# Kernel tuning notes

Measured on AMD Instinct MI355X. Metric: run time of the kernel, lower is better.

## Reference

```python
import jax, jax.numpy as jnp
import numpy as np

WS = (5, 5, 5, 5)  # 4D window

def _rel_index(ws):
    # faithful port of WindowAttention.relative_bias_4d
    coords = np.stack(np.meshgrid(*[np.arange(w) for w in ws], indexing='ij'))  # (4, H,W,Hs,Ws)
    flat = coords.reshape(len(ws), -1)                       # (4, N)
    rel = (flat[:, :, None] - flat[:, None, :]).transpose(1, 2, 0).astype(np.int64)  # (N, N, 4)
    rel = rel + np.array([ws[0] - 1, ws[1] - 1, ws[2] - 1, ws[3] - 1])
    rel[..., 0] *= (2 * ws[0] - 1) ** 3
    rel[..., 1] *= (2 * ws[1] - 1) ** 2
    rel[..., 2] *= (2 * ws[2] - 1)
    return rel.sum(-1)  # (N, N), values in [0, (2w-1)^4)


def setup_inputs() -> dict:
    key = jax.random.key(0)
    ks = jax.random.split(key, 7)
    dim, heads = 128, 4
    B_, nW = 64, 32
    N = 5 ** 4  # 625
    tbl = (2 * 5 - 1) ** 4  # 6561
    inp = {
        'x': jax.random.normal(ks[0], (B_, N, dim), jnp.float32),
        'mask': jax.random.normal(ks[1], (nW, N, N), jnp.float32),
        'qkv_w': jax.random.normal(ks[2], (3 * dim, dim), jnp.float32) * 0.02,
        'qkv_b': jax.random.normal(ks[3], (3 * dim,), jnp.float32) * 0.02,
        'proj_w': jax.random.normal(ks[4], (dim, dim), jnp.float32) * 0.02,
        'proj_b': jax.random.normal(ks[5], (dim,), jnp.float32) * 0.02,
        'bias_table': jax.random.normal(ks[6], (tbl, heads), jnp.float32) * 0.02,
        'rel_index': jnp.asarray(_rel_index(WS), jnp.int32),
    }
    return inp


def reference(x, mask, qkv_w, qkv_b, proj_w, proj_b, bias_table, rel_index):
    B_, N, C = x.shape
    H = bias_table.shape[-1]
    D = C // H
    scale = D ** -0.5
    # qkv projection -> (3, B_, H, N, D)
    qkv = (x @ qkv_w.T + qkv_b).reshape(B_, N, 3, H, D).transpose(2, 0, 3, 1, 4)
    q, k, v = qkv[0], qkv[1], qkv[2]
    attn = jnp.einsum('bhnd,bhmd->bhnm', q * scale, k)       # (B_, H, N, N)
    bias = bias_table[rel_index].transpose(2, 0, 1)          # (H, N, N)
    attn = attn + bias[None]
    nW = mask.shape[0]
    attn = attn.reshape(B_ // nW, nW, H, N, N) + mask[None, :, None]
    attn = jax.nn.softmax(attn.reshape(B_, H, N, N), axis=-1)
    out = jnp.einsum('bhnm,bhmd->bhnd', attn, v)             # (B_, H, N, D)
    out = out.transpose(0, 2, 1, 3).reshape(B_, N, C)
    return out @ proj_w.T + proj_b
```

## Files before the change

kernel.cpp:

```cpp
#include <hip/hip_runtime.h>
#include <stdint.h>

typedef __attribute__((ext_vector_type(8))) __bf16 bf16x8;
typedef __attribute__((ext_vector_type(4))) __bf16 bf16x4;
typedef __attribute__((ext_vector_type(4))) float f32x4;

#define DEV __device__ __forceinline__
#define LOG2E 1.4426950408889634f
#define SCALE 0.17677669529663687f

static constexpr size_t OFF_Q     = 0;
static constexpr size_t OFF_K     = 10485760;
static constexpr size_t OFF_VT    = 20971520;
static constexpr size_t OFF_O     = 31457280;
static constexpr size_t OFF_BIASP = 41697280;
static constexpr size_t OFF_WBF   = 44974080;

DEV bf16x8 cvt8(const float* p) {
  f32x4 a = *(const f32x4*)p;
  f32x4 b = *(const f32x4*)(p + 4);
  bf16x8 r;
  r[0]=(__bf16)a[0]; r[1]=(__bf16)a[1]; r[2]=(__bf16)a[2]; r[3]=(__bf16)a[3];
  r[4]=(__bf16)b[0]; r[5]=(__bf16)b[1]; r[6]=(__bf16)b[2]; r[7]=(__bf16)b[3];
  return r;
}

DEV f32x4 mfma16(bf16x8 a, bf16x8 b, f32x4 c) {
  return __builtin_amdgcn_mfma_f32_16x16x32_bf16(a, b, c, 0, 0, 0);
}

__global__ __launch_bounds__(256) void k_prep(const float* __restrict__ table,
                                              const int* __restrict__ rel,
                                              __bf16* __restrict__ bp,
                                              __bf16* __restrict__ qp,
                                              __bf16* __restrict__ kp,
                                              __bf16* __restrict__ vp,
                                              const float* __restrict__ wq,
                                              const float* __restrict__ wp,
                                              __bf16* __restrict__ wbf) {
  int blk = blockIdx.x;
  if (blk < 1600) {
    int t = blk * 256 + threadIdx.x;
    int h = t / 102400, rem = t % 102400;
    int i = rem / 160, q = rem % 160;
    int e0 = q * 4;
    int tile = e0 >> 5;
    int ein = e0 & 31;
    int g = ein >> 3, s0 = ein & 7;
    bf16x4 v;
    #pragma unroll
    for (int s2 = 0; s2 < 4; ++s2) {
      int s = s0 + s2;
      int col = 4 * g + (s < 4 ? s : s + 12);
      int j = tile * 32 + col;
      v[s2] = (i < 625 && j < 625)
                ? (__bf16)(table[(size_t)rel[(size_t)i * 625 + j] * 4 + h] * LOG2E)
                : (__bf16)0.f;
    }
    *(bf16x4*)(bp + ((size_t)h * 640 + i) * 640 + e0) = v;
  } else if (blk < 2560) {
    int t = (blk - 1600) * 256 + threadIdx.x;
    const int PAD1 = 256 * 15 * 32;
    if (t < PAD1) {
      int bh = t / 480, rem = t % 480;
      int row = 625 + rem / 32, d = rem & 31;
      size_t idx = ((size_t)bh * 640 + row) * 32 + d;
      qp[idx] = (__bf16)0.f;
      kp[idx] = (__bf16)0.f;
    } else {
      t -= PAD1;
      if (t < PAD1) {
        int bh = t / 480, rem = t % 480;
        int d = rem / 15, col = 625 + rem % 15;
        vp[((size_t)bh * 32 + d) * 640 + col] = (__bf16)0.f;
      }
    }
  } else {
    int t = (blk - 2560) * 256 + threadIdx.x;
    if (t < 49152) wbf[t] = (__bf16)wq[t];
    else           wbf[t] = (__bf16)wp[t - 49152];
  }
}

__global__ __launch_bounds__(256) void k_qkv(const float* __restrict__ x,
                                             const __bf16* __restrict__ wbf,
                                             const float* __restrict__ bias,
                                             __bf16* __restrict__ qp,
                                             __bf16* __restrict__ kp,
                                             __bf16* __restrict__ vp) {
  int lane = threadIdx.x & 63, wv = threadIdx.x >> 6;
  int g = lane >> 4, l15 = lane & 15;
  int row0 = (blockIdx.x * 4 + wv) * 16;

  bf16x8 a[4];
  #pragma unroll
  for (int ks = 0; ks < 4; ++ks)
    a[ks] = cvt8(x + (size_t)(row0 + l15) * 128 + ks * 32 + g * 8);

  #pragma unroll 1
  for (int nf = 0; nf < 24; ++nf) {
    f32x4 acc = {0.f, 0.f, 0.f, 0.f};
    int col = nf * 16 + l15;
    #pragma unroll
    for (int ks = 0; ks < 4; ++ks) {
      bf16x8 bfr = *(const bf16x8*)(wbf + (size_t)col * 128 + ks * 32 + g * 8);
      acc = mfma16(a[ks], bfr, acc);
    }
    float bv = bias[col];
    int which = nf >> 3;
    int h = (col >> 5) & 3, d = col & 31;
    #pragma unroll
    for (int r = 0; r < 4; ++r) {
      int row = row0 + 4 * g + r;
      int b_ = row / 625;
      int n = row - b_ * 625;
      float v = acc[r] + bv;
      size_t bh = (size_t)b_ * 4 + h;
      if (which == 0)       qp[(bh * 640 + n) * 32 + d] = (__bf16)(v * (SCALE * LOG2E));
      else if (which == 1)  kp[(bh * 640 + n) * 32 + d] = (__bf16)v;
      else                  vp[(bh * 32 + d) * 640 + n] = (__bf16)v;
    }
  }
}

__global__ __launch_bounds__(256, 4) void k_attn11(const __bf16* __restrict__ qball,
                                                   const __bf16* __restrict__ kball,
                                                   const __bf16* __restrict__ vball,
                                                   const __bf16* __restrict__ biasp,
                                                   const float* __restrict__ maskraw,
                                                   const __bf16* __restrict__ pw,
                                                   const float* __restrict__ pb,
                                                   float* __restrict__ out) {
  __shared__ __align__(16) unsigned short Pl[4][32 * 56];
  __shared__ __align__(16) __bf16 Osh[32 * 136];

  const int tid = threadIdx.x;
  const int lane = tid & 63, wv = tid >> 6;
  const int g = lane >> 4, l15 = lane & 15;

  const int bid = blockIdx.x;
  const int xcd = bid & 7, s = bid >> 3;
  const int w = xcd + 8 * (s & 3);
  const int r_ = s >> 2;
  const int o = r_ & 1, chunk = r_ >> 1;
  const int b = o * 32 + w;
  const int h = wv;
  const size_t bh = (size_t)b * 4 + h;
  const int i0 = chunk * 32;

  const __bf16* qp = qball + bh * (640 * 32);
  const __bf16* kp = kball + bh * (640 * 32);
  const __bf16* vp = vball + bh * (32 * 640);
  const float* maskw = maskraw + (size_t)w * 390625;

  const __bf16* kbase  = kp + (size_t)l15 * 32 + g * 8;
  const __bf16* vbase0 = vp + (size_t)l15 * 640 + 8 * g;
  const __bf16* vbase1 = vp + (size_t)(16 + l15) * 640 + 8 * g;
  const __bf16* brow0  = biasp + (size_t)h * 409600 + (size_t)(i0 + l15) * 640 + g * 8;
  const __bf16* brow1  = brow0 + 16 * 640;

  int ia = i0 + l15;       const int ir0 = ia < 625 ? ia : 624;
  int ib_ = i0 + 16 + l15; const int ir1 = ib_ < 625 ? ib_ : 624;
  const float* mrow0 = maskw + (size_t)ir0 * 625 + 4 * g;
  const float* mrow1 = maskw + (size_t)ir1 * 625 + 4 * g;

  bf16x8 aq0 = *(const bf16x8*)(qp + (size_t)(i0 + l15) * 32 + g * 8);
  bf16x8 aq1 = *(const bf16x8*)(qp + (size_t)(i0 + 16 + l15) * 32 + g * 8);

  unsigned short* Prow0 = &Pl[wv][l15 * 56];
  unsigned short* Prow1 = &Pl[wv][(16 + l15) * 56];

  f32x4 O00 = {0,0,0,0}, O01 = {0,0,0,0}, O10 = {0,0,0,0}, O11 = {0,0,0,0};
  float L0 = 0.f, L1 = 0.f;

  bf16x8 K0, K1;
  bf16x8 B0, B1;
  f32x4 C00, C01, C10, C11;

  C00 = *(const f32x4*)(mrow0);
  C01 = *(const f32x4*)(mrow0 + 16);
  C10 = *(const f32x4*)(mrow1);
  C11 = *(const f32x4*)(mrow1 + 16);
  K0  = *(const bf16x8*)(kbase);
  K1  = *(const bf16x8*)(kbase + 512);
  B0  = *(const bf16x8*)(brow0);
  B1  = *(const bf16x8*)(brow1);

  #pragma unroll 1
  for (int t = 0; t < 19; ++t) {
    bf16x8 v0 = *(const bf16x8*)(vbase0 + t * 32);
    bf16x8 v1 = *(const bf16x8*)(vbase1 + t * 32);
    f32x4 c00, c01, c10, c11;
    #pragma unroll
    for (int r = 0; r < 4; ++r) {
      c00[r] = fmaf(C00[r], LOG2E, (float)B0[r]);
      c01[r] = fmaf(C01[r], LOG2E, (float)B0[4 + r]);
      c10[r] = fmaf(C10[r], LOG2E, (float)B1[r]);
      c11[r] = fmaf(C11[r], LOG2E, (float)B1[4 + r]);
    }
    f32x4 S00 = mfma16(K0, aq0, c00);
    f32x4 S01 = mfma16(K1, aq0, c01);
    f32x4 S10 = mfma16(K0, aq1, c10);
    f32x4 S11 = mfma16(K1, aq1, c11);
    if (t < 18) {
      C00 = *(const f32x4*)(mrow0 + (t + 1) * 32);
      C01 = *(const f32x4*)(mrow0 + (t + 1) * 32 + 16);
      C10 = *(const f32x4*)(mrow1 + (t + 1) * 32);
      C11 = *(const f32x4*)(mrow1 + (t + 1) * 32 + 16);
    }
    K0 = *(const bf16x8*)(kbase + (size_t)(t + 1) * 1024);
    K1 = *(const bf16x8*)(kbase + (size_t)(t + 1) * 1024 + 512);
    B0 = *(const bf16x8*)(brow0 + (t + 1) * 32);
    B1 = *(const bf16x8*)(brow1 + (t + 1) * 32);

    float ps0 = 0.f, ps1 = 0.f;
    bf16x4 pk00, pk01, pk10, pk11;
    #pragma unroll
    for (int r = 0; r < 4; ++r) {
      float p00 = exp2f(S00[r]);
      float p01 = exp2f(S01[r]);
      float p10 = exp2f(S10[r]);
      float p11 = exp2f(S11[r]);
      ps0 += p00 + p01;
      ps1 += p10 + p11;
      pk00[r] = (__bf16)p00;
      pk01[r] = (__bf16)p01;
      pk10[r] = (__bf16)p10;
      pk11[r] = (__bf16)p11;
    }
    L0 += ps0; L1 += ps1;
    *(bf16x4*)(Prow0 + 4 * g) = pk00;
    *(bf16x4*)(Prow0 + 16 + 4 * g) = pk01;
    *(bf16x4*)(Prow1 + 4 * g) = pk10;
    *(bf16x4*)(Prow1 + 16 + 4 * g) = pk11;
    bf16x8 pa0 = *(const bf16x8*)(Prow0 + 8 * g);
    bf16x8 pa1 = *(const bf16x8*)(Prow1 + 8 * g);
    O00 = mfma16(pa0, v0, O00);
    O01 = mfma16(pa0, v1, O01);
    O10 = mfma16(pa1, v0, O10);
    O11 = mfma16(pa1, v1, O11);
  }

  {
    bf16x8 v0 = *(const bf16x8*)(vbase0 + 19 * 32);
    bf16x8 v1 = *(const bf16x8*)(vbase1 + 19 * 32);
    const float* mr0 = maskw + (size_t)ir0 * 625;
    const float* mr1 = maskw + (size_t)ir1 * 625;
    f32x4 c, S00, S01, S10, S11;
    #pragma unroll
    for (int r = 0; r < 4; ++r)
      c[r] = fmaf(mr0[608 + 4 * g + r], LOG2E, (float)B0[r]);
    S00 = mfma16(K0, aq0, c);
    #pragma unroll
    for (int r = 0; r < 4; ++r) {
      int j = 624 + 4 * g + r;
      c[r] = (j < 625) ? fmaf(mr0[j], LOG2E, (float)B0[4 + r]) : -1.0e30f;
    }
    S01 = mfma16(K1, aq0, c);
    #pragma unroll
    for (int r = 0; r < 4; ++r)
      c[r] = fmaf(mr1[608 + 4 * g + r], LOG2E, (float)B1[r]);
    S10 = mfma16(K0, aq1, c);
    #pragma unroll
    for (int r = 0; r < 4; ++r) {
      int j = 624 + 4 * g + r;
      c[r] = (j < 625) ? fmaf(mr1[j], LOG2E, (float)B1[4 + r]) : -1.0e30f;
    }
    S11 = mfma16(K1, aq1, c);

    float ps0 = 0.f, ps1 = 0.f;
    bf16x4 pk00, pk01, pk10, pk11;
    #pragma unroll
    for (int r = 0; r < 4; ++r) {
      float p00 = exp2f(S00[r]);
      float p01 = exp2f(S01[r]);
      float p10 = exp2f(S10[r]);
      float p11 = exp2f(S11[r]);
      ps0 += p00 + p01;
      ps1 += p10 + p11;
      pk00[r] = (__bf16)p00;
      pk01[r] = (__bf16)p01;
      pk10[r] = (__bf16)p10;
      pk11[r] = (__bf16)p11;
    }
    L0 += ps0; L1 += ps1;
    *(bf16x4*)(Prow0 + 4 * g) = pk00;
    *(bf16x4*)(Prow0 + 16 + 4 * g) = pk01;
    *(bf16x4*)(Prow1 + 4 * g) = pk10;
    *(bf16x4*)(Prow1 + 16 + 4 * g) = pk11;
    bf16x8 pa0 = *(const bf16x8*)(Prow0 + 8 * g);
    bf16x8 pa1 = *(const bf16x8*)(Prow1 + 8 * g);
    O00 = mfma16(pa0, v0, O00);
    O01 = mfma16(pa0, v1, O01);
    O10 = mfma16(pa1, v0, O10);
    O11 = mfma16(pa1, v1, O11);
  }

  L0 += __shfl_xor(L0, 16); L0 += __shfl_xor(L0, 32);
  L1 += __shfl_xor(L1, 16); L1 += __shfl_xor(L1, 32);
  float inv0 = 1.0f / L0, inv1 = 1.0f / L1;
  f32x4 iv0, iv1;
  #pragma unroll
  for (int r = 0; r < 4; ++r) {
    iv0[r] = __shfl(inv0, 4 * g + r);
    iv1[r] = __shfl(inv1, 4 * g + r);
  }
  #pragma unroll
  for (int r = 0; r < 4; ++r) {
    Osh[(4 * g + r) * 136 + 32 * h + l15]           = (__bf16)(O00[r] * iv0[r]);
    Osh[(4 * g + r) * 136 + 32 * h + 16 + l15]      = (__bf16)(O01[r] * iv0[r]);
    Osh[(16 + 4 * g + r) * 136 + 32 * h + l15]      = (__bf16)(O10[r] * iv1[r]);
    Osh[(16 + 4 * g + r) * 136 + 32 * h + 16 + l15] = (__bf16)(O11[r] * iv1[r]);
  }
  __syncthreads();

  bf16x8 a2[2][4];
  #pragma unroll
  for (int m = 0; m < 2; ++m)
    #pragma unroll
    for (int ks = 0; ks < 4; ++ks)
      a2[m][ks] = *(const bf16x8*)&Osh[(m * 16 + l15) * 136 + ks * 32 + g * 8];

  #pragma unroll
  for (int n = 0; n < 2; ++n) {
    const int col = 32 * h + n * 16 + l15;
    bf16x8 bw[4];
    #pragma unroll
    for (int ks = 0; ks < 4; ++ks)
      bw[ks] = *(const bf16x8*)(pw + (size_t)col * 128 + ks * 32 + g * 8);
    float bv = pb[col];
    #pragma unroll
    for (int m = 0; m < 2; ++m) {
      f32x4 acc = {0.f, 0.f, 0.f, 0.f};
      #pragma unroll
      for (int ks = 0; ks < 4; ++ks)
        acc = mfma16(a2[m][ks], bw[ks], acc);
      #pragma unroll
      for (int r = 0; r < 4; ++r) {
        int irow = i0 + m * 16 + 4 * g + r;
        if (irow < 625)
          out[((size_t)b * 625 + irow) * 128 + col] = acc[r] + bv;
      }
    }
  }
}

extern "C" void kernel_launch(void* const* d_in, const int* in_sizes, int n_in,
                              void* d_out, int out_size, void* d_ws, size_t ws_size,
                              hipStream_t stream) {
  (void)in_sizes; (void)n_in; (void)out_size; (void)ws_size;
  const float* x      = (const float*)d_in[0];
  const float* mask   = (const float*)d_in[1];
  const float* qkv_w  = (const float*)d_in[2];
  const float* qkv_b  = (const float*)d_in[3];
  const float* proj_w = (const float*)d_in[4];
  const float* proj_b = (const float*)d_in[5];
  const float* table  = (const float*)d_in[6];
  const int*   rel    = (const int*)d_in[7];
  char* ws = (char*)d_ws;
  float* out = (float*)d_out;

  __bf16* qp    = (__bf16*)(ws + OFF_Q);
  __bf16* kp    = (__bf16*)(ws + OFF_K);
  __bf16* vp    = (__bf16*)(ws + OFF_VT);
  __bf16* biasp = (__bf16*)(ws + OFF_BIASP);
  __bf16* wbf   = (__bf16*)(ws + OFF_WBF);

  k_prep<<<2816, 256, 0, stream>>>(table, rel, biasp, qp, kp, vp, qkv_w, proj_w, wbf);
  k_qkv<<<625, 256, 0, stream>>>(x, wbf, qkv_b, qp, kp, vp);
  k_attn11<<<1280, 256, 0, stream>>>(qp, kp, vp, biasp, mask, wbf + 49152, proj_b, out);
}
```

Before: 146.9 us.

## Split attention key range across two wave groups per head and combine partials

The attention kernel doubles its block size to 512 threads so that two waves per head each process half of the 20 key tiles (split-K). Partial O accumulators and row sums from the second half are passed through shared memory and added into the first half's before normalization. The output projection is then spread over all 8 waves. This shortens the serial per-wave loop and adds latency hiding, at the cost of an extra shared-memory combine, added barriers and tighter register limits under launch_bounds(512, 8).

```diff
diff --git a/kernel.cpp b/kernel.cpp
--- a/kernel.cpp
+++ b/kernel.cpp
@@ -12,7 +12,6 @@
 static constexpr size_t OFF_Q     = 0;
 static constexpr size_t OFF_K     = 10485760;
 static constexpr size_t OFF_VT    = 20971520;
-static constexpr size_t OFF_O     = 31457280;
 static constexpr size_t OFF_BIASP = 41697280;
 static constexpr size_t OFF_WBF   = 44974080;
 
@@ -123,7 +122,7 @@
   }
 }
 
-__global__ __launch_bounds__(256, 4) void k_attn11(const __bf16* __restrict__ qball,
+__global__ __launch_bounds__(512, 8) void k_attn12(const __bf16* __restrict__ qball,
                                                    const __bf16* __restrict__ kball,
                                                    const __bf16* __restrict__ vball,
                                                    const __bf16* __restrict__ biasp,
@@ -131,12 +130,13 @@
                                                    const __bf16* __restrict__ pw,
                                                    const float* __restrict__ pb,
                                                    float* __restrict__ out) {
-  __shared__ __align__(16) unsigned short Pl[4][32 * 56];
-  __shared__ __align__(16) __bf16 Osh[32 * 136];
+  __shared__ __align__(16) char arena[28672];
 
   const int tid = threadIdx.x;
   const int lane = tid & 63, wv = tid >> 6;
   const int g = lane >> 4, l15 = lane & 15;
+  const int h = wv & 3, jh = wv >> 2;
+  const int tbase = jh * 10;
 
   const int bid = blockIdx.x;
   const int xcd = bid & 7, s = bid >> 3;
@@ -144,7 +144,6 @@
   const int r_ = s >> 2;
   const int o = r_ & 1, chunk = r_ >> 1;
   const int b = o * 32 + w;
-  const int h = wv;
   const size_t bh = (size_t)b * 4 + h;
   const int i0 = chunk * 32;
 
@@ -167,8 +166,8 @@
   bf16x8 aq0 = *(const bf16x8*)(qp + (size_t)(i0 + l15) * 32 + g * 8);
   bf16x8 aq1 = *(const bf16x8*)(qp + (size_t)(i0 + 16 + l15) * 32 + g * 8);
 
-  unsigned short* Prow0 = &Pl[wv][l15 * 56];
-  unsigned short* Prow1 = &Pl[wv][(16 + l15) * 56];
+  unsigned short* Prow0 = (unsigned short*)arena + wv * (32 * 56) + l15 * 56;
+  unsigned short* Prow1 = (unsigned short*)arena + wv * (32 * 56) + (16 + l15) * 56;
 
   f32x4 O00 = {0,0,0,0}, O01 = {0,0,0,0}, O10 = {0,0,0,0}, O11 = {0,0,0,0};
   float L0 = 0.f, L1 = 0.f;
@@ -177,41 +176,104 @@
   bf16x8 B0, B1;
   f32x4 C00, C01, C10, C11;
 
-  C00 = *(const f32x4*)(mrow0);
-  C01 = *(const f32x4*)(mrow0 + 16);
-  C10 = *(const f32x4*)(mrow1);
-  C11 = *(const f32x4*)(mrow1 + 16);
-  K0  = *(const bf16x8*)(kbase);
-  K1  = *(const bf16x8*)(kbase + 512);
-  B0  = *(const bf16x8*)(brow0);
-  B1  = *(const bf16x8*)(brow1);
+  C00 = *(const f32x4*)(mrow0 + tbase * 32);
+  C01 = *(const f32x4*)(mrow0 + tbase * 32 + 16);
+  C10 = *(const f32x4*)(mrow1 + tbase * 32);
+  C11 = *(const f32x4*)(mrow1 + tbase * 32 + 16);
+  K0  = *(const bf16x8*)(kbase + (size_t)tbase * 1024);
+  K1  = *(const bf16x8*)(kbase + (size_t)tbase * 1024 + 512);
+  B0  = *(const bf16x8*)(brow0 + tbase * 32);
+  B1  = *(const bf16x8*)(brow1 + tbase * 32);
+
+#define BODY(T, DOPREF)                                                        \
+  {                                                                            \
+    bf16x8 v0 = *(const bf16x8*)(vbase0 + (T) * 32);                           \
+    bf16x8 v1 = *(const bf16x8*)(vbase1 + (T) * 32);                           \
+    f32x4 c00, c01, c10, c11;                                                  \
+    _Pragma("unroll")                                                          \
+    for (int r = 0; r < 4; ++r) {                                              \
+      c00[r] = fmaf(C00[r], LOG2E, (float)B0[r]);                              \
+      c01[r] = fmaf(C01[r], LOG2E, (float)B0[4 + r]);                          \
+      c10[r] = fmaf(C10[r], LOG2E, (float)B1[r]);                              \
+      c11[r] = fmaf(C11[r], LOG2E, (float)B1[4 + r]);                          \
+    }                                                                          \
+    f32x4 S00 = mfma16(K0, aq0, c00);                                          \
+    f32x4 S01 = mfma16(K1, aq0, c01);                                          \
+    f32x4 S10 = mfma16(K0, aq1, c10);                                          \
+    f32x4 S11 = mfma16(K1, aq1, c11);                                          \
+    if (DOPREF) {                                                              \
+      if ((T) < 18) {                                                          \
+        C00 = *(const f32x4*)(mrow0 + ((T) + 1) * 32);                         \
+        C01 = *(const f32x4*)(mrow0 + ((T) + 1) * 32 + 16);                    \
+        C10 = *(const f32x4*)(mrow1 + ((T) + 1) * 32);                         \
+        C11 = *(const f32x4*)(mrow1 + ((T) + 1) * 32 + 16);                    \
+      }                                                                        \
+      K0 = *(const bf16x8*)(kbase + (size_t)((T) + 1) * 1024);                 \
+      K1 = *(const bf16x8*)(kbase + (size_t)((T) + 1) * 1024 + 512);           \
+      B0 = *(const bf16x8*)(brow0 + ((T) + 1) * 32);                           \
+      B1 = *(const bf16x8*)(brow1 + ((T) + 1) * 32);                           \
+    }                                                                          \
+    float ps0 = 0.f, ps1 = 0.f;                                                \
+    bf16x4 pk00, pk01, pk10, pk11;                                             \
+    _Pragma("unroll")                                                          \
+    for (int r = 0; r < 4; ++r) {                                              \
+      float p00 = exp2f(S00[r]);                                               \
+      float p01 = exp2f(S01[r]);                                               \
+      float p10 = exp2f(S10[r]);                                               \
+      float p11 = exp2f(S11[r]);                                               \
+      ps0 += p00 + p01;                                                        \
+      ps1 += p10 + p11;                                                        \
+      pk00[r] = (__bf16)p00;                                                   \
+      pk01[r] = (__bf16)p01;                                                   \
+      pk10[r] = (__bf16)p10;                                                   \
+      pk11[r] = (__bf16)p11;                                                   \
+    }                                                                          \
+    L0 += ps0; L1 += ps1;                                                      \
+    *(bf16x4*)(Prow0 + 4 * g) = pk00;                                          \
+    *(bf16x4*)(Prow0 + 16 + 4 * g) = pk01;                                     \
+    *(bf16x4*)(Prow1 + 4 * g) = pk10;                                          \
+    *(bf16x4*)(Prow1 + 16 + 4 * g) = pk11;                                     \
+    bf16x8 pa0 = *(const bf16x8*)(Prow0 + 8 * g);                              \
+    bf16x8 pa1 = *(const bf16x8*)(Prow1 + 8 * g);                              \
+    O00 = mfma16(pa0, v0, O00);                                                \
+    O01 = mfma16(pa0, v1, O01);                                                \
+    O10 = mfma16(pa1, v0, O10);                                                \
+    O11 = mfma16(pa1, v1, O11);                                                \
+  }
 
   #pragma unroll 1
-  for (int t = 0; t < 19; ++t) {
-    bf16x8 v0 = *(const bf16x8*)(vbase0 + t * 32);
-    bf16x8 v1 = *(const bf16x8*)(vbase1 + t * 32);
-    f32x4 c00, c01, c10, c11;
-    #pragma unroll
-    for (int r = 0; r < 4; ++r) {
-      c00[r] = fmaf(C00[r], LOG2E, (float)B0[r]);
-      c01[r] = fmaf(C01[r], LOG2E, (float)B0[4 + r]);
-      c10[r] = fmaf(C10[r], LOG2E, (float)B1[r]);
-      c11[r] = fmaf(C11[r], LOG2E, (float)B1[4 + r]);
-    }
-    f32x4 S00 = mfma16(K0, aq0, c00);
-    f32x4 S01 = mfma16(K1, aq0, c01);
-    f32x4 S10 = mfma16(K0, aq1, c10);
-    f32x4 S11 = mfma16(K1, aq1, c11);
-    if (t < 18) {
-      C00 = *(const f32x4*)(mrow0 + (t + 1) * 32);
-      C01 = *(const f32x4*)(mrow0 + (t + 1) * 32 + 16);
-      C10 = *(const f32x4*)(mrow1 + (t + 1) * 32);
-      C11 = *(const f32x4*)(mrow1 + (t + 1) * 32 + 16);
-    }
-    K0 = *(const bf16x8*)(kbase + (size_t)(t + 1) * 1024);
-    K1 = *(const bf16x8*)(kbase + (size_t)(t + 1) * 1024 + 512);
-    B0 = *(const bf16x8*)(brow0 + (t + 1) * 32);
-    B1 = *(const bf16x8*)(brow1 + (t + 1) * 32);
+  for (int t = tbase; t < tbase + 9; ++t) {
+    BODY(t, 1)
+  }
+
+  if (jh == 0) {
+    BODY(9, 0)
+  } else {
+    bf16x8 v0 = *(const bf16x8*)(vbase0 + 19 * 32);
+    bf16x8 v1 = *(const bf16x8*)(vbase1 + 19 * 32);
+    const float* mr0 = maskw + (size_t)ir0 * 625;
+    const float* mr1 = maskw + (size_t)ir1 * 625;
+    f32x4 c, S00, S01, S10, S11;
+    #pragma unroll
+    for (int r = 0; r < 4; ++r)
+      c[r] = fmaf(mr0[608 + 4 * g + r], LOG2E, (float)B0[r]);
+    S00 = mfma16(K0, aq0, c);
+    #pragma unroll
+    for (int r = 0; r < 4; ++r) {
+      int j = 624 + 4 * g + r;
+      c[r] = (j < 625) ? fmaf(mr0[j], LOG2E, (float)B0[4 + r]) : -1.0e30f;
+    }
+    S01 = mfma16(K1, aq0, c);
+    #pragma unroll
+    for (int r = 0; r < 4; ++r)
+      c[r] = fmaf(mr1[608 + 4 * g + r], LOG2E, (float)B1[r]);
+    S10 = mfma16(K0, aq1, c);
+    #pragma unroll
+    for (int r = 0; r < 4; ++r) {
+      int j = 624 + 4 * g + r;
+      c[r] = (j < 625) ? fmaf(mr1[j], LOG2E, (float)B1[4 + r]) : -1.0e30f;
+    }
+    S11 = mfma16(K1, aq1, c);
 
     float ps0 = 0.f, ps1 = 0.f;
     bf16x4 pk00, pk01, pk10, pk11;
@@ -240,77 +302,54 @@
     O10 = mfma16(pa1, v0, O10);
     O11 = mfma16(pa1, v1, O11);
   }
-
-  {
-    bf16x8 v0 = *(const bf16x8*)(vbase0 + 19 * 32);
-    bf16x8 v1 = *(const bf16x8*)(vbase1 + 19 * 32);
-    const float* mr0 = maskw + (size_t)ir0 * 625;
-    const float* mr1 = maskw + (size_t)ir1 * 625;
-    f32x4 c, S00, S01, S10, S11;
-    #pragma unroll
-    for (int r = 0; r < 4; ++r)
-      c[r] = fmaf(mr0[608 + 4 * g + r], LOG2E, (float)B0[r]);
-    S00 = mfma16(K0, aq0, c);
-    #pragma unroll
-    for (int r = 0; r < 4; ++r) {
-      int j = 624 + 4 * g + r;
-      c[r] = (j < 625) ? fmaf(mr0[j], LOG2E, (float)B0[4 + r]) : -1.0e30f;
-    }
-    S01 = mfma16(K1, aq0, c);
-    #pragma unroll
-    for (int r = 0; r < 4; ++r)
-      c[r] = fmaf(mr1[608 + 4 * g + r], LOG2E, (float)B1[r]);
-    S10 = mfma16(K0, aq1, c);
-    #pragma unroll
-    for (int r = 0; r < 4; ++r) {
-      int j = 624 + 4 * g + r;
-      c[r] = (j < 625) ? fmaf(mr1[j], LOG2E, (float)B1[4 + r]) : -1.0e30f;
-    }
-    S11 = mfma16(K1, aq1, c);
-
-    float ps0 = 0.f, ps1 = 0.f;
-    bf16x4 pk00, pk01, pk10, pk11;
-    #pragma unroll
-    for (int r = 0; r < 4; ++r) {
-      float p00 = exp2f(S00[r]);
-      float p01 = exp2f(S01[r]);
-      float p10 = exp2f(S10[r]);
-      float p11 = exp2f(S11[r]);
-      ps0 += p00 + p01;
-      ps1 += p10 + p11;
-      pk00[r] = (__bf16)p00;
-      pk01[r] = (__bf16)p01;
-      pk10[r] = (__bf16)p10;
-      pk11[r] = (__bf16)p11;
-    }
-    L0 += ps0; L1 += ps1;
-    *(bf16x4*)(Prow0 + 4 * g) = pk00;
-    *(bf16x4*)(Prow0 + 16 + 4 * g) = pk01;
-    *(bf16x4*)(Prow1 + 4 * g) = pk10;
-    *(bf16x4*)(Prow1 + 16 + 4 * g) = pk11;
-    bf16x8 pa0 = *(const bf16x8*)(Prow0 + 8 * g);
-    bf16x8 pa1 = *(const bf16x8*)(Prow1 + 8 * g);
-    O00 = mfma16(pa0, v0, O00);
-    O01 = mfma16(pa0, v1, O01);
-    O10 = mfma16(pa1, v0, O10);
-    O11 = mfma16(pa1, v1, O11);
-  }
-
-  L0 += __shfl_xor(L0, 16); L0 += __shfl_xor(L0, 32);
-  L1 += __shfl_xor(L1, 16); L1 += __shfl_xor(L1, 32);
-  float inv0 = 1.0f / L0, inv1 = 1.0f / L1;
-  f32x4 iv0, iv1;
-  #pragma unroll
-  for (int r = 0; r < 4; ++r) {
-    iv0[r] = __shfl(inv0, 4 * g + r);
-    iv1[r] = __shfl(inv1, 4 * g + r);
-  }
-  #pragma unroll
-  for (int r = 0; r < 4; ++r) {
-    Osh[(4 * g + r) * 136 + 32 * h + l15]           = (__bf16)(O00[r] * iv0[r]);
-    Osh[(4 * g + r) * 136 + 32 * h + 16 + l15]      = (__bf16)(O01[r] * iv0[r]);
-    Osh[(16 + 4 * g + r) * 136 + 32 * h + l15]      = (__bf16)(O10[r] * iv1[r]);
-    Osh[(16 + 4 * g + r) * 136 + 32 * h + 16 + l15] = (__bf16)(O11[r] * iv1[r]);
+#undef BODY
+
+  __syncthreads();
+  float* comb = (float*)arena;
+  __bf16* Osh = (__bf16*)(arena + 18432);
+
+  if (jh == 1) {
+    float* dst = comb + ((size_t)h * 64 + lane) * 18;
+    #pragma unroll
+    for (int r = 0; r < 4; ++r) {
+      dst[r]      = O00[r];
+      dst[4 + r]  = O01[r];
+      dst[8 + r]  = O10[r];
+      dst[12 + r] = O11[r];
+    }
+    dst[16] = L0;
+    dst[17] = L1;
+  }
+  __syncthreads();
+
+  if (jh == 0) {
+    const float* src = comb + ((size_t)h * 64 + lane) * 18;
+    #pragma unroll
+    for (int r = 0; r < 4; ++r) {
+      O00[r] += src[r];
+      O01[r] += src[4 + r];
+      O10[r] += src[8 + r];
+      O11[r] += src[12 + r];
+    }
+    L0 += src[16];
+    L1 += src[17];
+
+    L0 += __shfl_xor(L0, 16); L0 += __shfl_xor(L0, 32);
+    L1 += __shfl_xor(L1, 16); L1 += __shfl_xor(L1, 32);
+    float inv0 = 1.0f / L0, inv1 = 1.0f / L1;
+    f32x4 iv0, iv1;
+    #pragma unroll
+    for (int r = 0; r < 4; ++r) {
+      iv0[r] = __shfl(inv0, 4 * g + r);
+      iv1[r] = __shfl(inv1, 4 * g + r);
+    }
+    #pragma unroll
+    for (int r = 0; r < 4; ++r) {
+      Osh[(4 * g + r) * 136 + 32 * h + l15]           = (__bf16)(O00[r] * iv0[r]);
+      Osh[(4 * g + r) * 136 + 32 * h + 16 + l15]      = (__bf16)(O01[r] * iv0[r]);
+      Osh[(16 + 4 * g + r) * 136 + 32 * h + l15]      = (__bf16)(O10[r] * iv1[r]);
+      Osh[(16 + 4 * g + r) * 136 + 32 * h + 16 + l15] = (__bf16)(O11[r] * iv1[r]);
+    }
   }
   __syncthreads();
 
@@ -321,9 +360,8 @@
     for (int ks = 0; ks < 4; ++ks)
       a2[m][ks] = *(const bf16x8*)&Osh[(m * 16 + l15) * 136 + ks * 32 + g * 8];
 
-  #pragma unroll
-  for (int n = 0; n < 2; ++n) {
-    const int col = 32 * h + n * 16 + l15;
+  {
+    const int col = 16 * wv + l15;
     bf16x8 bw[4];
     #pragma unroll
     for (int ks = 0; ks < 4; ++ks)
@@ -368,5 +406,5 @@
 
   k_prep<<<2816, 256, 0, stream>>>(table, rel, biasp, qp, kp, vp, qkv_w, proj_w, wbf);
   k_qkv<<<625, 256, 0, stream>>>(x, wbf, qkv_b, qp, kp, vp);
-  k_attn11<<<1280, 256, 0, stream>>>(qp, kp, vp, biasp, mask, wbf + 49152, proj_b, out);
-}
+  k_attn12<<<1280, 512, 0, stream>>>(qp, kp, vp, biasp, mask, wbf + 49152, proj_b, out);
+}
```

Result: slower. 355.0 us (+141.7%).
